# Performance work log

Hardware: AMD Instinct MI355X
Metric: run time of the kernel (lower is better)

Reference implementation:

```python
import jax, jax.numpy as jnp
import numpy as np

NUM_EXPERTS = 8
D_MODEL = 768
D_FF = 4 * D_MODEL


def setup_inputs() -> dict:
    key = jax.random.key(0)
    ks = jax.random.split(key, 7)
    s = 0.02
    x = jax.random.normal(ks[0], (2, 1024, D_MODEL), dtype=jnp.float32)
    router_w = jax.random.normal(ks[1], (D_MODEL, NUM_EXPERTS), dtype=jnp.float32) * s
    router_b = jnp.zeros((NUM_EXPERTS,), dtype=jnp.float32)
    w1 = jax.random.normal(ks[2], (NUM_EXPERTS, D_MODEL, D_FF), dtype=jnp.float32) * s
    b1 = jnp.zeros((NUM_EXPERTS, D_FF), dtype=jnp.float32)
    w2 = jax.random.normal(ks[3], (NUM_EXPERTS, D_FF, D_MODEL), dtype=jnp.float32) * s
    b2 = jnp.zeros((NUM_EXPERTS, D_MODEL), dtype=jnp.float32)
    return {"x": x, "router_w": router_w, "router_b": router_b,
            "w1": w1, "b1": b1, "w2": w2, "b2": b2}


def reference(x, router_w, router_b, w1, b1, w2, b2):
    B, S, D = x.shape
    x_flat = x.reshape(-1, D)                      # [T, D]
    logits = x_flat @ router_w + router_b          # [T, E]
    probs = jax.nn.softmax(logits, axis=-1)
    expert_idx = jnp.argmax(probs, axis=-1)        # [T] int, top-1 routing
    onehot = jax.nn.one_hot(expert_idx, NUM_EXPERTS, dtype=x.dtype)  # [T, E]

    # Per-expert FFN; combine via top-1 one-hot (output is NOT scaled by prob,
    # matching the original). Dropout is eval-mode identity.
    out = jnp.zeros_like(x_flat)
    for e in range(NUM_EXPERTS):
        h = jax.nn.relu(x_flat @ w1[e] + b1[e])    # [T, D_FF]
        y = h @ w2[e] + b2[e]                      # [T, D]
        out = out + onehot[:, e:e + 1] * y
    outputs = out.reshape(B, S, D)

    # Load-balance loss: MSE between empirical expert usage and uniform.
    usage = jnp.bincount(expert_idx, length=NUM_EXPERTS).astype(jnp.float32)
    usage = usage / usage.sum()
    uniform = jnp.full((NUM_EXPERTS,), 1.0 / NUM_EXPERTS, dtype=jnp.float32)
    load_balance_loss = jnp.mean((usage - uniform) ** 2)
    return outputs, load_balance_loss
```

## Files before the change

### kernel.cpp

```cpp
#include <hip/hip_runtime.h>
#include <hip/hip_bf16.h>

#define NTOK 2048
#define DMODEL 768
#define DFF 3072
#define NEXP 8
#define MAXT 40

typedef short bf16x8 __attribute__((ext_vector_type(8)));
typedef float f32x4 __attribute__((ext_vector_type(4)));

typedef __attribute__((address_space(1))) const char GCHAR;
typedef __attribute__((address_space(3))) char LCHAR;
#define GL16(g, l) __builtin_amdgcn_global_load_lds((GCHAR*)(g), (LCHAR*)(l), 16, 0, 0)

template <int K, int N>
__device__ void transpose32(const float* __restrict__ W, __hip_bfloat16* __restrict__ WT,
                            int e, int k0, int n0, float* T) {
  const int t = threadIdx.x;
#pragma unroll
  for (int i = 0; i < 2; i++) {
    const int idx = t + i * 256;
    const int kr = idx >> 4;
    const int c4 = (idx & 15) * 4;
    float4 v = *(const float4*)(W + ((size_t)e * K + k0 + kr) * N + n0 + c4);
    T[kr * 65 + c4 + 0] = v.x;
    T[kr * 65 + c4 + 1] = v.y;
    T[kr * 65 + c4 + 2] = v.z;
    T[kr * 65 + c4 + 3] = v.w;
  }
  __syncthreads();
  const int n = t >> 2;
  const int kc = (t & 3) * 8;
  __align__(16) __hip_bfloat16 u[8];
#pragma unroll
  for (int j = 0; j < 8; j++) u[j] = __float2bfloat16(T[(kc + j) * 65 + n]);
  *(int4*)(WT + ((size_t)e * N + n0 + n) * K + k0 + kc) = *(const int4*)u;
}

__global__ __launch_bounds__(256, 4) void k_router_t1(
    const float* __restrict__ x, const float* __restrict__ rw,
    const float* __restrict__ rb, __hip_bfloat16* __restrict__ xbf,
    int* __restrict__ eidx, int* __restrict__ cnt,
    const float* __restrict__ w1, __hip_bfloat16* __restrict__ wT1) {
  __shared__ float T[32 * 65];
  if (blockIdx.x >= 512) {
    int tb = blockIdx.x - 512;
    int n_i = tb % (DFF / 64);
    int k_i = (tb / (DFF / 64)) % (DMODEL / 32);
    int e = tb / ((DFF / 64) * (DMODEL / 32));
    transpose32<DMODEL, DFF>(w1, wT1, e, k_i * 32, n_i * 64, T);
    return;
  }
  int tok = (blockIdx.x * blockDim.x + threadIdx.x) >> 6;
  int lane = threadIdx.x & 63;
  if (tok >= NTOK) return;
  const float* xr = x + (size_t)tok * DMODEL;
  double acc[NEXP];
#pragma unroll
  for (int e = 0; e < NEXP; e++) acc[e] = 0.0;
  for (int d0 = 0; d0 < DMODEL; d0 += 64) {
    float v = xr[d0 + lane];
    xbf[(size_t)tok * DMODEL + d0 + lane] = __float2bfloat16(v);
    const float* wrow = rw + (size_t)(d0 + lane) * NEXP;
#pragma unroll
    for (int e = 0; e < NEXP; e++) acc[e] += (double)v * (double)wrow[e];
  }
#pragma unroll
  for (int e = 0; e < NEXP; e++) {
    double a = acc[e];
#pragma unroll
    for (int s = 32; s > 0; s >>= 1) a += __shfl_xor(a, s);
    acc[e] = a;
  }
  if (lane == 0) {
    int best = 0;
    double bv = acc[0] + (double)rb[0];
#pragma unroll
    for (int e = 1; e < NEXP; e++) {
      double v = acc[e] + (double)rb[e];
      if (v > bv) { bv = v; best = e; }
    }
    eidx[tok] = best;
    atomicAdd(&cnt[best], 1);
  }
}

__global__ void k_scan(const int* __restrict__ cnt, int* __restrict__ off,
                       int* __restrict__ cur, float* __restrict__ loss,
                       int* __restrict__ tiles, int* __restrict__ ntile) {
  if (threadIdx.x == 0) {
    int s = 0;
    float l = 0.f;
    int nt = 0;
    for (int e = 0; e < NEXP; e++) {
      off[e] = s;
      cur[e] = s;
      for (int m = 0; m < cnt[e]; m += 64) tiles[nt++] = (e << 20) | m;
      s += cnt[e];
      float u = (float)cnt[e] / (float)NTOK - 1.0f / (float)NEXP;
      l += u * u;
    }
    *ntile = nt;
    *loss = l / (float)NEXP;
  }
}

__global__ __launch_bounds__(256) void k_build(const int* __restrict__ eidx,
                                               int* __restrict__ cur,
                                               int* __restrict__ list) {
  int t = blockIdx.x * blockDim.x + threadIdx.x;
  if (t < NTOK) {
    int e = eidx[t];
    int p = atomicAdd(&cur[e], 1);
    list[p] = t;
  }
}

template <int K_TOT, int KCHUNK, int N, int NSPLIT, bool RELU_BF16, bool GATHER_A,
          int TK, int TN>
__global__ __launch_bounds__(256, 8) void k_gemm8(
    const __hip_bfloat16* __restrict__ A, const __hip_bfloat16* __restrict__ BT,
    const float* __restrict__ bias, void* __restrict__ Cout,
    const int* __restrict__ cnt, const int* __restrict__ off,
    const int* __restrict__ list, const int* __restrict__ tiles,
    const int* __restrict__ ntile, const float* __restrict__ Tsrc,
    __hip_bfloat16* __restrict__ Tdst) {
  constexpr int NX = N / 64;
  constexpr int W = NX * MAXT * NSPLIT;
  constexpr int NT = KCHUNK / 32;
  __shared__ __align__(16) char smem[8448];

  if constexpr (TK > 0) {
    if (blockIdx.x >= W) {
      int tb = blockIdx.x - W;
      int n_i = tb % (TN / 64);
      int k_i = (tb / (TN / 64)) % (TK / 32);
      int e = tb / ((TN / 64) * (TK / 32));
      transpose32<TK, TN>(Tsrc, Tdst, e, k_i * 32, n_i * 64, (float*)smem);
      return;
    }
  }

  int b = blockIdx.x;
  constexpr int q = W / 8, r = W % 8;
  const int xcd = b & 7, ii = b >> 3;
  const int widx = (xcd < r ? xcd * (q + 1) : r * (q + 1) + (xcd - r) * q) + ii;
  const int split = widx % NSPLIT;
  const int rest = widx / NSPLIT;
  const int ti = rest % MAXT;
  const int nx = rest / MAXT;
  if (ti >= *ntile) return;
  const int tv = tiles[ti];
  const int e = tv >> 20;
  const int m0 = tv & 0xFFFFF;
  const int ce = cnt[e];
  const int oe = off[e];
  const int n0 = nx * 64;
  const int kbase = split * KCHUNK;

  const int tid = threadIdx.x;
  const int lane = tid & 63;
  const int w = tid >> 6;
  const int wr = (w >> 1) * 32;
  const int wc = (w & 1) * 32;
  const int fr = lane & 15;
  const int hi = lane >> 4;
  const int xr = (fr >> 1) & 3;

  const int srow = tid >> 2;
  const int cch = (tid & 3) ^ ((tid >> 3) & 3);

  const __hip_bfloat16* ga;
  {
    int mr = m0 + srow;
    int src;
    if (GATHER_A) {
      src = list[oe + (mr < ce ? mr : 0)];
    } else {
      int p2 = oe + mr;
      src = p2 < NTOK ? p2 : NTOK - 1;
    }
    ga = A + (size_t)src * K_TOT + kbase + cch * 8;
  }
  const __hip_bfloat16* gb = BT + ((size_t)e * N + n0 + srow) * K_TOT + kbase + cch * 8;

  char* lA = smem + tid * 16;
  char* lB = smem + 4096 + tid * 16;

  f32x4 acc[2][2] = {};

#pragma unroll 1
  for (int t = 0; t < NT; ++t) {
    GL16(ga + t * 32, lA);
    GL16(gb + t * 32, lB);
    __syncthreads();
    {
      bf16x8 fa[2], fb[2];
#pragma unroll
      for (int mf = 0; mf < 2; mf++) {
        const int row = wr + mf * 16 + fr;
        fa[mf] = *(const bf16x8*)(smem + row * 64 + ((hi ^ xr) * 16));
      }
#pragma unroll
      for (int nf = 0; nf < 2; nf++) {
        const int row = wc + nf * 16 + fr;
        fb[nf] = *(const bf16x8*)(smem + 4096 + row * 64 + ((hi ^ xr) * 16));
      }
#pragma unroll
      for (int mf = 0; mf < 2; mf++)
#pragma unroll
        for (int nf = 0; nf < 2; nf++)
          acc[mf][nf] = __builtin_amdgcn_mfma_f32_16x16x32_bf16(fa[mf], fb[nf],
                                                                acc[mf][nf], 0, 0, 0);
    }
    __syncthreads();
  }

#pragma unroll
  for (int mf = 0; mf < 2; mf++) {
#pragma unroll
    for (int jj = 0; jj < 4; jj++) {
      const int mloc = m0 + wr + mf * 16 + hi * 4 + jj;
      if (mloc >= ce) continue;
      if (RELU_BF16) {
        __hip_bfloat16* C = (__hip_bfloat16*)Cout;
        size_t row = (size_t)(oe + mloc) * N;
        const float* bi = bias + (size_t)e * N;
#pragma unroll
        for (int nf = 0; nf < 2; nf++) {
          int nn = n0 + wc + nf * 16 + fr;
          float v = acc[mf][nf][jj] + bi[nn];
          C[row + nn] = __float2bfloat16(v > 0.f ? v : 0.f);
        }
      } else {
        float* C = (float*)Cout;
        int tok = list[oe + mloc];
        size_t row = ((size_t)split * NTOK + tok) * N;
#pragma unroll
        for (int nf = 0; nf < 2; nf++) {
          int nn = n0 + wc + nf * 16 + fr;
          C[row + nn] = acc[mf][nf][jj];
        }
      }
    }
  }
}

__global__ __launch_bounds__(256) void k_reduce(const float* __restrict__ p,
                                                const float* __restrict__ b2,
                                                const int* __restrict__ eidx,
                                                float* __restrict__ out) {
  const int idx = blockIdx.x * 256 + threadIdx.x;
  const int base = idx * 4;
  const int tok = base / DMODEL;
  const int n = base - tok * DMODEL;
  const int e = eidx[tok];
  float4 a = *(const float4*)(p + (size_t)0 * NTOK * DMODEL + base);
  float4 c = *(const float4*)(p + (size_t)1 * NTOK * DMODEL + base);
  float4 d = *(const float4*)(p + (size_t)2 * NTOK * DMODEL + base);
  float4 g = *(const float4*)(p + (size_t)3 * NTOK * DMODEL + base);
  float4 bb = *(const float4*)(b2 + (size_t)e * DMODEL + n);
  float4 o;
  o.x = a.x + c.x + d.x + g.x + bb.x;
  o.y = a.y + c.y + d.y + g.y + bb.y;
  o.z = a.z + c.z + d.z + g.z + bb.z;
  o.w = a.w + c.w + d.w + g.w + bb.w;
  *(float4*)(out + base) = o;
}

template <int K, int N, bool RELU_BF16, bool GATHER_A, bool SCATTER_C>
__global__ __launch_bounds__(256) void k_gemm(
    const __hip_bfloat16* __restrict__ A, const float* __restrict__ Bw,
    const float* __restrict__ bias, void* __restrict__ Cout,
    const int* __restrict__ cnt, const int* __restrict__ off,
    const int* __restrict__ list) {
  const int e = blockIdx.z;
  const int ce = cnt[e];
  const int m0 = blockIdx.y * 128;
  if (m0 >= ce) return;
  const int oe = off[e];
  const int n0 = blockIdx.x * 128;

  __shared__ __hip_bfloat16 Asm[128][32];
  __shared__ __hip_bfloat16 Bsm[128][32];

  const int tid = threadIdx.x;
  const int ra = tid >> 1;
  const int ha = (tid & 1) * 16;
  size_t arow;
  {
    int mr = m0 + ra;
    int src;
    if (GATHER_A) {
      src = (mr < ce) ? list[oe + mr] : list[oe];
    } else {
      int p = oe + mr;
      src = (p < NTOK) ? p : (NTOK - 1);
    }
    arow = (size_t)src * K;
  }
  const int rbk = tid >> 3;
  const int nb = (tid & 7) * 16;
  const float* bsrc0 = Bw + ((size_t)e * K + rbk) * N + n0 + nb;

  const int w = tid >> 6;
  const int lane = tid & 63;
  const int wr = (w >> 1) * 64;
  const int wc = (w & 1) * 64;
  const int fr = lane & 15;
  const int fk = (lane >> 4) * 8;

  f32x4 acc[4][4] = {};

  for (int k0 = 0; k0 < K; k0 += 32) {
    __syncthreads();
    {
      const __hip_bfloat16* s = A + arow + k0 + ha;
      int4 v0 = *(const int4*)(s);
      int4 v1 = *(const int4*)(s + 8);
      *(int4*)(&Asm[ra][ha]) = v0;
      *(int4*)(&Asm[ra][ha + 8]) = v1;
    }
    {
      const float* s = bsrc0 + (size_t)k0 * N;
      float4 q0 = *(const float4*)(s);
      float4 q1 = *(const float4*)(s + 4);
      float4 q2 = *(const float4*)(s + 8);
      float4 q3 = *(const float4*)(s + 12);
      __hip_bfloat16* dst = &Bsm[nb][0] + rbk;
      dst[0 * 32] = __float2bfloat16(q0.x);
      dst[1 * 32] = __float2bfloat16(q0.y);
      dst[2 * 32] = __float2bfloat16(q0.z);
      dst[3 * 32] = __float2bfloat16(q0.w);
      dst[4 * 32] = __float2bfloat16(q1.x);
      dst[5 * 32] = __float2bfloat16(q1.y);
      dst[6 * 32] = __float2bfloat16(q1.z);
      dst[7 * 32] = __float2bfloat16(q1.w);
      dst[8 * 32] = __float2bfloat16(q2.x);
      dst[9 * 32] = __float2bfloat16(q2.y);
      dst[10 * 32] = __float2bfloat16(q2.z);
      dst[11 * 32] = __float2bfloat16(q2.w);
      dst[12 * 32] = __float2bfloat16(q3.x);
      dst[13 * 32] = __float2bfloat16(q3.y);
      dst[14 * 32] = __float2bfloat16(q3.z);
      dst[15 * 32] = __float2bfloat16(q3.w);
    }
    __syncthreads();

    bf16x8 fa[4], fb[4];
#pragma unroll
    for (int mf = 0; mf < 4; mf++) fa[mf] = *(const bf16x8*)(&Asm[wr + mf * 16 + fr][fk]);
#pragma unroll
    for (int nf = 0; nf < 4; nf++) fb[nf] = *(const bf16x8*)(&Bsm[wc + nf * 16 + fr][fk]);
#pragma unroll
    for (int mf = 0; mf < 4; mf++)
#pragma unroll
      for (int nf = 0; nf < 4; nf++)
        acc[mf][nf] = __builtin_amdgcn_mfma_f32_16x16x32_bf16(fa[mf], fb[nf], acc[mf][nf], 0, 0, 0);
  }

#pragma unroll
  for (int mf = 0; mf < 4; mf++) {
#pragma unroll
    for (int j = 0; j < 4; j++) {
      const int mloc = m0 + wr + mf * 16 + (lane >> 4) * 4 + j;
      if (mloc >= ce) continue;
      if (RELU_BF16) {
        __hip_bfloat16* C = (__hip_bfloat16*)Cout;
        size_t row = (size_t)(oe + mloc) * N;
        const float* bi = bias + (size_t)e * N;
#pragma unroll
        for (int nf = 0; nf < 4; nf++) {
          int nn = n0 + wc + nf * 16 + fr;
          float v = acc[mf][nf][j] + bi[nn];
          C[row + nn] = __float2bfloat16(v > 0.f ? v : 0.f);
        }
      } else {
        float* C = (float*)Cout;
        int tok = SCATTER_C ? list[oe + mloc] : (oe + mloc);
        size_t row = (size_t)tok * N;
        const float* bi = bias + (size_t)e * N;
#pragma unroll
        for (int nf = 0; nf < 4; nf++) {
          int nn = n0 + wc + nf * 16 + fr;
          C[row + nn] = acc[mf][nf][j] + bi[nn];
        }
      }
    }
  }
}

extern "C" void kernel_launch(void* const* d_in, const int* in_sizes, int n_in,
                              void* d_out, int out_size, void* d_ws, size_t ws_size,
                              hipStream_t stream) {
  const float* x = (const float*)d_in[0];
  const float* rw = (const float*)d_in[1];
  const float* rb = (const float*)d_in[2];
  const float* w1 = (const float*)d_in[3];
  const float* b1 = (const float*)d_in[4];
  const float* w2 = (const float*)d_in[5];
  const float* b2 = (const float*)d_in[6];
  float* out = (float*)d_out;

  char* ws = (char*)d_ws;
  int* cnt = (int*)(ws + 0);
  int* off = (int*)(ws + 32);
  int* cur = (int*)(ws + 64);
  int* ntile = (int*)(ws + 96);
  int* tiles = (int*)(ws + 128);
  int* eidx = (int*)(ws + 512);
  int* list = (int*)(ws + 8704);
  __hip_bfloat16* xbf = (__hip_bfloat16*)(ws + 65536);
  __hip_bfloat16* h = (__hip_bfloat16*)(ws + 4194304);
  __hip_bfloat16* wT1 = (__hip_bfloat16*)(ws + 20971520);
  float* part = (float*)(ws + 20971520);
  __hip_bfloat16* wT2 = (__hip_bfloat16*)(ws + 58720256);

  float* loss = out + (size_t)2 * 1024 * 768;
  const size_t REQ = 58720256ull + 37748736ull;

  (void)hipMemsetAsync(cnt, 0, 96, stream);
  if (ws_size < REQ)
    (void)hipMemsetAsync(d_out, 0, (size_t)out_size * sizeof(float), stream);

  if (ws_size >= REQ) {
    const int T1BLK = (DMODEL / 32) * (DFF / 64) * NEXP;
    const int T2BLK = (DFF / 32) * (DMODEL / 64) * NEXP;
    k_router_t1<<<512 + T1BLK, 256, 0, stream>>>(x, rw, rb, xbf, eidx, cnt, w1, wT1);
    k_scan<<<1, 64, 0, stream>>>(cnt, off, cur, loss, tiles, ntile);
    k_build<<<8, 256, 0, stream>>>(eidx, cur, list);
    k_gemm8<DMODEL, DMODEL, DFF, 1, true, true, DFF, DMODEL>
        <<<(DFF / 64) * MAXT + T2BLK, 256, 0, stream>>>(
            xbf, wT1, b1, h, cnt, off, list, tiles, ntile, w2, wT2);
    k_gemm8<DFF, DFF / 4, DMODEL, 4, false, false, 0, 64>
        <<<(DMODEL / 64) * MAXT * 4, 256, 0, stream>>>(
            h, wT2, nullptr, part, cnt, off, list, tiles, ntile, nullptr, nullptr);
    k_reduce<<<(NTOK * DMODEL) / 1024, 256, 0, stream>>>(part, b2, eidx, out);
  } else {
    k_router_t1<<<512, 256, 0, stream>>>(x, rw, rb, xbf, eidx, cnt, w1, nullptr);
    k_scan<<<1, 64, 0, stream>>>(cnt, off, cur, loss, tiles, ntile);
    k_build<<<8, 256, 0, stream>>>(eidx, cur, list);
    k_gemm<DMODEL, DFF, true, true, false>
        <<<dim3(DFF / 128, 16, NEXP), 256, 0, stream>>>(xbf, w1, b1, h, cnt, off, list);
    k_gemm<DFF, DMODEL, false, false, true>
        <<<dim3(DMODEL / 128, 16, NEXP), 256, 0, stream>>>(h, w2, b2, out, cnt, off, list);
  }
}
```

Measured before the change: 158.0 us.

## Widen GEMM tile to 128 columns and double-buffer LDS loads

The expert GEMM kernel now computes 64x128 output tiles per block instead of 64x64, so each wave holds 2x4 MFMA accumulators. The A tile is reused across twice as many columns and half as many blocks are launched. It also double-buffers the LDS staging, issuing the next K-slice's global-to-LDS loads before computing the current one, with explicit vmcnt waits and raw barriers. The cost is more LDS and registers per block (launch bounds lowered to 6) and fewer blocks to fill the GPU.

New measurement: 140.8 us. 1.12x faster.

```diff
diff --git a/kernel.cpp b/kernel.cpp
--- a/kernel.cpp
+++ b/kernel.cpp
@@ -119,17 +119,17 @@
 
 template <int K_TOT, int KCHUNK, int N, int NSPLIT, bool RELU_BF16, bool GATHER_A,
           int TK, int TN>
-__global__ __launch_bounds__(256, 8) void k_gemm8(
+__global__ __launch_bounds__(256, 6) void k_gemm9(
     const __hip_bfloat16* __restrict__ A, const __hip_bfloat16* __restrict__ BT,
     const float* __restrict__ bias, void* __restrict__ Cout,
     const int* __restrict__ cnt, const int* __restrict__ off,
     const int* __restrict__ list, const int* __restrict__ tiles,
     const int* __restrict__ ntile, const float* __restrict__ Tsrc,
     __hip_bfloat16* __restrict__ Tdst) {
-  constexpr int NX = N / 64;
+  constexpr int NX = N / 128;
   constexpr int W = NX * MAXT * NSPLIT;
   constexpr int NT = KCHUNK / 32;
-  __shared__ __align__(16) char smem[8448];
+  __shared__ __align__(16) char smem[24576];
 
   if constexpr (TK > 0) {
     if (blockIdx.x >= W) {
@@ -156,14 +156,14 @@
   const int m0 = tv & 0xFFFFF;
   const int ce = cnt[e];
   const int oe = off[e];
-  const int n0 = nx * 64;
+  const int n0 = nx * 128;
   const int kbase = split * KCHUNK;
 
   const int tid = threadIdx.x;
   const int lane = tid & 63;
   const int w = tid >> 6;
   const int wr = (w >> 1) * 32;
-  const int wc = (w & 1) * 32;
+  const int wc = (w & 1) * 64;
   const int fr = lane & 15;
   const int hi = lane >> 4;
   const int xr = (fr >> 1) & 3;
@@ -183,39 +183,56 @@
     }
     ga = A + (size_t)src * K_TOT + kbase + cch * 8;
   }
-  const __hip_bfloat16* gb = BT + ((size_t)e * N + n0 + srow) * K_TOT + kbase + cch * 8;
-
-  char* lA = smem + tid * 16;
-  char* lB = smem + 4096 + tid * 16;
-
-  f32x4 acc[2][2] = {};
-
+  const __hip_bfloat16* gb[2];
+#pragma unroll
+  for (int j = 0; j < 2; j++) {
+    int nr = n0 + j * 64 + srow;
+    gb[j] = BT + ((size_t)e * N + nr) * K_TOT + kbase + cch * 8;
+  }
+
+  f32x4 acc[2][4] = {};
+
+#define STAGE(buf, kc)                                              \
+  do {                                                              \
+    GL16(ga + (kc), smem + (buf)*4096 + tid * 16);                  \
+    GL16(gb[0] + (kc), smem + 8192 + (buf)*8192 + tid * 16);        \
+    GL16(gb[1] + (kc), smem + 8192 + (buf)*8192 + 4096 + tid * 16); \
+  } while (0)
+
+  STAGE(0, 0);
 #pragma unroll 1
   for (int t = 0; t < NT; ++t) {
-    GL16(ga + t * 32, lA);
-    GL16(gb + t * 32, lB);
-    __syncthreads();
+    if (t + 1 < NT) {
+      STAGE((t + 1) & 1, (t + 1) * 32);
+      asm volatile("s_waitcnt vmcnt(3)" ::: "memory");
+    } else {
+      asm volatile("s_waitcnt vmcnt(0)" ::: "memory");
+    }
+    __builtin_amdgcn_s_barrier();
     {
-      bf16x8 fa[2], fb[2];
+      const char* bA = smem + (t & 1) * 4096;
+      const char* bB = smem + 8192 + (t & 1) * 8192;
+      bf16x8 fa[2], fb[4];
 #pragma unroll
       for (int mf = 0; mf < 2; mf++) {
         const int row = wr + mf * 16 + fr;
-        fa[mf] = *(const bf16x8*)(smem + row * 64 + ((hi ^ xr) * 16));
+        fa[mf] = *(const bf16x8*)(bA + row * 64 + ((hi ^ xr) * 16));
       }
 #pragma unroll
-      for (int nf = 0; nf < 2; nf++) {
+      for (int nf = 0; nf < 4; nf++) {
         const int row = wc + nf * 16 + fr;
-        fb[nf] = *(const bf16x8*)(smem + 4096 + row * 64 + ((hi ^ xr) * 16));
+        fb[nf] = *(const bf16x8*)(bB + row * 64 + ((hi ^ xr) * 16));
       }
 #pragma unroll
       for (int mf = 0; mf < 2; mf++)
 #pragma unroll
-        for (int nf = 0; nf < 2; nf++)
+        for (int nf = 0; nf < 4; nf++)
           acc[mf][nf] = __builtin_amdgcn_mfma_f32_16x16x32_bf16(fa[mf], fb[nf],
                                                                 acc[mf][nf], 0, 0, 0);
     }
-    __syncthreads();
-  }
+    __builtin_amdgcn_s_barrier();
+  }
+#undef STAGE
 
 #pragma unroll
   for (int mf = 0; mf < 2; mf++) {
@@ -228,7 +245,7 @@
         size_t row = (size_t)(oe + mloc) * N;
         const float* bi = bias + (size_t)e * N;
 #pragma unroll
-        for (int nf = 0; nf < 2; nf++) {
+        for (int nf = 0; nf < 4; nf++) {
           int nn = n0 + wc + nf * 16 + fr;
           float v = acc[mf][nf][jj] + bi[nn];
           C[row + nn] = __float2bfloat16(v > 0.f ? v : 0.f);
@@ -238,7 +255,7 @@
         int tok = list[oe + mloc];
         size_t row = ((size_t)split * NTOK + tok) * N;
 #pragma unroll
-        for (int nf = 0; nf < 2; nf++) {
+        for (int nf = 0; nf < 4; nf++) {
           int nn = n0 + wc + nf * 16 + fr;
           C[row + nn] = acc[mf][nf][jj];
         }
@@ -430,11 +447,11 @@
     k_router_t1<<<512 + T1BLK, 256, 0, stream>>>(x, rw, rb, xbf, eidx, cnt, w1, wT1);
     k_scan<<<1, 64, 0, stream>>>(cnt, off, cur, loss, tiles, ntile);
     k_build<<<8, 256, 0, stream>>>(eidx, cur, list);
-    k_gemm8<DMODEL, DMODEL, DFF, 1, true, true, DFF, DMODEL>
-        <<<(DFF / 64) * MAXT + T2BLK, 256, 0, stream>>>(
+    k_gemm9<DMODEL, DMODEL, DFF, 1, true, true, DFF, DMODEL>
+        <<<(DFF / 128) * MAXT + T2BLK, 256, 0, stream>>>(
             xbf, wT1, b1, h, cnt, off, list, tiles, ntile, w2, wT2);
-    k_gemm8<DFF, DFF / 4, DMODEL, 4, false, false, 0, 64>
-        <<<(DMODEL / 64) * MAXT * 4, 256, 0, stream>>>(
+    k_gemm9<DFF, DFF / 4, DMODEL, 4, false, false, 0, 64>
+        <<<(DMODEL / 128) * MAXT * 4, 256, 0, stream>>>(
             h, wT2, nullptr, part, cnt, off, list, tiles, ntile, nullptr, nullptr);
     k_reduce<<<(NTOK * DMODEL) / 1024, 256, 0, stream>>>(part, b2, eidx, out);
   } else {
```
